# Kernel tuning notes

Hardware: AMD Instinct MI355X
Metric: run time of the kernel (lower is better)

## Reference

```python
import jax, jax.numpy as jnp
import numpy as np
import math

B, N, C, H = 4, 8192, 256, 8
D = C // H
EPS = 1e-6

def _ln(x, g, b):
    m = jnp.mean(x, -1, keepdims=True)
    v = jnp.mean((x - m) ** 2, -1, keepdims=True)
    return (x - m) * jax.lax.rsqrt(v + EPS) * g + b

def _pe(n, c):
    # sinusoidal PE, sin at even dims, cos at odd dims
    pos = jnp.arange(n, dtype=jnp.float32)[:, None]
    div = jnp.exp(jnp.arange(0, c, 2, dtype=jnp.float32) * (-math.log(10000.0) / c))
    ang = pos * div  # [n, c//2]
    return jnp.stack([jnp.sin(ang), jnp.cos(ang)], axis=-1).reshape(n, c)

def _heads(t):
    b, n, _ = t.shape
    return t.reshape(b, n, H, D).transpose(0, 2, 1, 3)  # [B,H,N,D]

def _forward(input, fx, Input_f, ln1_g, ln1_b, ln2_g, ln2_b, ln3_g, ln3_b,
             Wq, bq, Wk0, bk0, Wv0, bv0, Wk1, bk1, Wv1, bv1, Wo, bo,
             Wm1, bm1, Wm2, bm2, mu):
    pe = _pe(N, C)
    x = input + pe
    f = Input_f + pe
    x = _ln(x, ln1_g, ln1_b)
    f = _ln(f, ln2_g, ln2_b)
    # LinearCrossAttention: query from f; (key,value) streams = [f, x]
    q = jax.nn.softmax(_heads(f @ Wq + bq), axis=-1)  # [B,H,N,D]
    out = q
    for src, Wk, bk, Wv, bv in ((f, Wk0, bk0, Wv0, bv0), (x, Wk1, bk1, Wv1, bv1)):
        k = jax.nn.softmax(_heads(src @ Wk + bk), axis=-1)
        v = _heads(src @ Wv + bv)
        kv = jnp.einsum('bhnd,bhne->bhde', k, v)   # [B,H,D,D] small
        ksum = jnp.sum(k, axis=2)                  # [B,H,D]
        d_inv = 1.0 / jnp.einsum('bhnd,bhd->bhn', q, ksum)[..., None]
        out = out + jnp.einsum('bhnd,bhde->bhne', q, kv) * d_inv
    out = out.transpose(0, 2, 1, 3).reshape(out.shape[0], N, C)
    x = out @ Wo + bo + input          # residual
    y = _ln(x, ln3_g, ln3_b)
    y = jax.nn.gelu(y @ Wm1 + bm1, approximate=False) @ Wm2 + bm2
    x = x + y
    # bilinear low-rank fx update without n x n matrix
    xtfx = jnp.einsum('bnc,bnf->bcf', x, fx)
    fx_new = jnp.einsum('bnc,bcf->bnf', x * jax.nn.softplus(mu), xtfx)
    fx_new = jnp.where(fx_new >= 0, fx_new, 0.01 * fx_new)  # LeakyReLU(0.01)
    return x, fx_new

def setup_inputs() -> dict:
    key = jax.random.key(0)
    ks = jax.random.split(key, 16)
    w = lambda i: jax.random.normal(ks[i], (C, C), jnp.float32) * 0.02
    z = jnp.zeros((C,), jnp.float32)
    o = jnp.ones((C,), jnp.float32)
    return {
        'input': jax.random.normal(ks[0], (B, N, C), jnp.float32),
        'fx': jax.random.normal(ks[1], (B, N, C), jnp.float32),
        'Input_f': jax.random.normal(ks[2], (B, N, C), jnp.float32),
        'ln1_g': o, 'ln1_b': z, 'ln2_g': o, 'ln2_b': z, 'ln3_g': o, 'ln3_b': z,
        'Wq': w(3), 'bq': z,
        'Wk0': w(4), 'bk0': z, 'Wv0': w(5), 'bv0': z,
        'Wk1': w(6), 'bk1': z, 'Wv1': w(7), 'bv1': z,
        'Wo': w(8), 'bo': z,
        'Wm1': w(9), 'bm1': z, 'Wm2': w(10), 'bm2': z,
        'mu': z,
    }

def reference(input, fx, Input_f, ln1_g, ln1_b, ln2_g, ln2_b, ln3_g, ln3_b,
              Wq, bq, Wk0, bk0, Wv0, bv0, Wk1, bk1, Wv1, bv1, Wo, bo,
              Wm1, bm1, Wm2, bm2, mu):
    return _forward(input, fx, Input_f, ln1_g, ln1_b, ln2_g, ln2_b, ln3_g, ln3_b,
                    Wq, bq, Wk0, bk0, Wv0, bv0, Wk1, bk1, Wv1, bv1, Wo, bo,
                    Wm1, bm1, Wm2, bm2, mu)
```

## Files before the change

kernel.cpp:

```cpp
#include <hip/hip_runtime.h>


typedef __attribute__((ext_vector_type(8))) short    bf16x8;
typedef __attribute__((ext_vector_type(4))) float    f32x4;
typedef __attribute__((ext_vector_type(8))) unsigned short ushortx8;
typedef __attribute__((ext_vector_type(4))) unsigned short ushortx4;

static constexpr int Bn = 4, Nn = 8192, Cn = 256, Hn = 8, Dn = 32;
static constexpr int BN = Bn * Nn;
static constexpr long long S = (long long)BN * Cn;

#define DEVI __device__ __forceinline__

#define GLOAD_LDS16(gsrc, ldst)                                                  \
    __builtin_amdgcn_global_load_lds(                                            \
        (const __attribute__((address_space(1))) unsigned int*)(gsrc),           \
        (__attribute__((address_space(3))) unsigned int*)(ldst), 16, 0, 0)

DEVI unsigned short f2bf(float f) {
    unsigned int u = __builtin_bit_cast(unsigned int, f);
    u += 0x7fffu + ((u >> 16) & 1u);
    return (unsigned short)(u >> 16);
}
DEVI float bf2f(unsigned short h) {
    unsigned int u = ((unsigned int)h) << 16;
    return __builtin_bit_cast(float, u);
}

__global__ __launch_bounds__(256) void wtrans_all_kernel(
    const float* __restrict__ W0, const float* __restrict__ W1,
    const float* __restrict__ W2, const float* __restrict__ W3,
    const float* __restrict__ W4, const float* __restrict__ W5,
    const float* __restrict__ W6, const float* __restrict__ W7,
    unsigned short* __restrict__ WtAll) {
    __shared__ float tile[256][33];
    const float* W;
    switch (blockIdx.y) {
        case 0: W = W0; break; case 1: W = W1; break;
        case 2: W = W2; break; case 3: W = W3; break;
        case 4: W = W4; break; case 5: W = W5; break;
        case 6: W = W6; break; default: W = W7; break;
    }
    unsigned short* Wt = WtAll + (size_t)blockIdx.y * 65536;
    int t = threadIdx.x;
    int j0 = blockIdx.x * 32;
#pragma unroll
    for (int p = 0; p < 32; ++p) {
        int k = p * 8 + (t >> 5);
        tile[k][t & 31] = W[k * Cn + j0 + (t & 31)];
    }
    __syncthreads();
#pragma unroll
    for (int p = 0; p < 8; ++p) {
        int j = p * 4 + (t >> 6);
        int k0 = (t & 63) * 4;
        ushortx4 o;
        o.x = f2bf(tile[k0 + 0][j]);
        o.y = f2bf(tile[k0 + 1][j]);
        o.z = f2bf(tile[k0 + 2][j]);
        o.w = f2bf(tile[k0 + 3][j]);
        *(ushortx4*)(Wt + (long long)(j0 + j) * Cn + k0) = o;
    }
}

__global__ __launch_bounds__(256) void peln2_kernel(
    const float* __restrict__ in0, const float* __restrict__ g0, const float* __restrict__ b0,
    unsigned short* __restrict__ o0,
    const float* __restrict__ in1, const float* __restrict__ g1, const float* __restrict__ b1,
    unsigned short* __restrict__ o1) {
    const float* in  = blockIdx.y ? in1 : in0;
    const float* gam = blockIdx.y ? g1 : g0;
    const float* bet = blockIdx.y ? b1 : b0;
    unsigned short* outb = blockIdx.y ? o1 : o0;
    int r = blockIdx.x * 4 + (threadIdx.x >> 6);
    int lane = threadIdx.x & 63;
    int n = r & (Nn - 1);
    int c0 = lane * 4;
    const float* rowp = in + (long long)r * Cn + c0;
    float v0 = rowp[0], v1 = rowp[1], v2 = rowp[2], v3 = rowp[3];
    const float Kf = 0.07195578415606394f;
    float fn = (float)n;
    float ang0 = fn * expf(-Kf * (float)(2 * lane));
    float ang1 = fn * expf(-Kf * (float)(2 * lane + 1));
    v0 += sinf(ang0); v1 += cosf(ang0);
    v2 += sinf(ang1); v3 += cosf(ang1);
    float s = v0 + v1 + v2 + v3;
#pragma unroll
    for (int m = 1; m < 64; m <<= 1) s += __shfl_xor(s, m, 64);
    float mean = s * (1.0f / 256.0f);
    float d0 = v0 - mean, d1 = v1 - mean, d2 = v2 - mean, d3 = v3 - mean;
    float q = d0 * d0 + d1 * d1 + d2 * d2 + d3 * d3;
#pragma unroll
    for (int m = 1; m < 64; m <<= 1) q += __shfl_xor(q, m, 64);
    float rstd = rsqrtf(q * (1.0f / 256.0f) + 1e-6f);
    float4 g4 = *(const float4*)(gam + c0);
    float4 b4 = *(const float4*)(bet + c0);
    ushortx4 o;
    o.x = f2bf(d0 * rstd * g4.x + b4.x);
    o.y = f2bf(d1 * rstd * g4.y + b4.y);
    o.z = f2bf(d2 * rstd * g4.z + b4.z);
    o.w = f2bf(d3 * rstd * g4.w + b4.w);
    *(ushortx4*)(outb + (long long)r * Cn + c0) = o;
}

__global__ __launch_bounds__(256) void ln_kernel(const float* __restrict__ in,
                                                 const float* __restrict__ gam,
                                                 const float* __restrict__ bet,
                                                 unsigned short* __restrict__ outb) {
    int r = blockIdx.x * 4 + (threadIdx.x >> 6);
    int lane = threadIdx.x & 63;
    int c0 = lane * 4;
    const float* rowp = in + (long long)r * Cn + c0;
    float v0 = rowp[0], v1 = rowp[1], v2 = rowp[2], v3 = rowp[3];
    float s = v0 + v1 + v2 + v3;
#pragma unroll
    for (int m = 1; m < 64; m <<= 1) s += __shfl_xor(s, m, 64);
    float mean = s * (1.0f / 256.0f);
    float d0 = v0 - mean, d1 = v1 - mean, d2 = v2 - mean, d3 = v3 - mean;
    float q = d0 * d0 + d1 * d1 + d2 * d2 + d3 * d3;
#pragma unroll
    for (int m = 1; m < 64; m <<= 1) q += __shfl_xor(q, m, 64);
    float rstd = rsqrtf(q * (1.0f / 256.0f) + 1e-6f);
    float4 g4 = *(const float4*)(gam + c0);
    float4 b4 = *(const float4*)(bet + c0);
    ushortx4 o;
    o.x = f2bf(d0 * rstd * g4.x + b4.x);
    o.y = f2bf(d1 * rstd * g4.y + b4.y);
    o.z = f2bf(d2 * rstd * g4.z + b4.z);
    o.w = f2bf(d3 * rstd * g4.w + b4.w);
    *(ushortx4*)(outb + (long long)r * Cn + c0) = o;
}

__global__ __launch_bounds__(256, 4) void qkv_gemm_kernel(
    const unsigned short* __restrict__ A0, const unsigned short* __restrict__ A1,
    const unsigned short* __restrict__ WtAll,
    const float* __restrict__ bq, const float* __restrict__ bk0,
    const float* __restrict__ bv0, const float* __restrict__ bk1,
    const float* __restrict__ bv1,
    unsigned short* __restrict__ qb, unsigned short* __restrict__ kb0,
    unsigned short* __restrict__ vb0, unsigned short* __restrict__ kb1,
    unsigned short* __restrict__ vb1,
    float* __restrict__ ks0, float* __restrict__ ks1) {
    __shared__ unsigned short As[2][128][64];
    int t = threadIdx.x;
    int row0 = blockIdx.x * 128;
    int y = blockIdx.y;

    const unsigned short* A;
    const unsigned short* Btw;
    const float* bsel; unsigned short* osel; bool sm; float* ksp;
    int colIn;
    if (y < 12) {
        A = A0; int wid = y >> 2; colIn = (y & 3) * 64;
        Btw = WtAll + (size_t)wid * 65536;
        if (wid == 0)      { bsel = bq;  osel = qb;  sm = true;  ksp = nullptr; }
        else if (wid == 1) { bsel = bk0; osel = kb0; sm = true;  ksp = ks0; }
        else               { bsel = bv0; osel = vb0; sm = false; ksp = nullptr; }
    } else {
        int y2 = y - 12;
        A = A1; int wid = y2 >> 2; colIn = (y2 & 3) * 64;
        Btw = WtAll + (size_t)(3 + wid) * 65536;
        if (wid == 0)      { bsel = bk1; osel = kb1; sm = true;  ksp = ks1; }
        else               { bsel = bv1; osel = vb1; sm = false; ksp = nullptr; }
    }

    int lane = t & 63, w = t >> 6;
    int wr = w >> 1, wc = w & 1;
    int frow = lane & 15, fk = (lane >> 4) * 8;

    bf16x8 bfr[4][2][2];
#pragma unroll
    for (int kt = 0; kt < 4; ++kt)
#pragma unroll
        for (int ks = 0; ks < 2; ++ks)
#pragma unroll
            for (int n = 0; n < 2; ++n)
                bfr[kt][ks][n] = *(const bf16x8*)(
                    Btw + (long long)(colIn + wc * 32 + n * 16 + frow) * Cn
                        + kt * 64 + ks * 32 + fk);

    int srow_in_g = lane >> 3;
    int schunk = lane & 7;
    auto stageA = [&](int kt, int bf) {
#pragma unroll
        for (int i = 0; i < 4; ++i) {
            int g = w * 4 + i;
            int r = g * 8 + srow_in_g;
            int c = schunk ^ (r & 7);
            const unsigned short* src = A + (long long)(row0 + r) * Cn + kt * 64 + c * 8;
            GLOAD_LDS16(src, &As[bf][g * 8][0]);
        }
    };

    f32x4 acc[4][2];
#pragma unroll
    for (int m = 0; m < 4; ++m)
#pragma unroll
        for (int n = 0; n < 2; ++n) {
            acc[m][n][0] = 0.f; acc[m][n][1] = 0.f;
            acc[m][n][2] = 0.f; acc[m][n][3] = 0.f;
        }

    stageA(0, 0);
    int bf = 0;
#pragma unroll
    for (int kt = 0; kt < 4; ++kt) {
        if (kt < 3) {
            stageA(kt + 1, bf ^ 1);
            asm volatile("s_waitcnt vmcnt(4)" ::: "memory");
        } else {
            asm volatile("s_waitcnt vmcnt(0)" ::: "memory");
        }
        __builtin_amdgcn_s_barrier();
#pragma unroll
        for (int ks = 0; ks < 2; ++ks) {
#pragma unroll
            for (int m = 0; m < 4; ++m) {
                int arow = wr * 64 + m * 16 + frow;
                bf16x8 afr = *(const bf16x8*)&As[bf][arow][(ks * 32 + fk) ^ ((arow & 7) << 3)];
#pragma unroll
                for (int n = 0; n < 2; ++n)
                    acc[m][n] = __builtin_amdgcn_mfma_f32_16x16x32_bf16(afr, bfr[kt][ks][n],
                                                                        acc[m][n], 0, 0, 0);
            }
        }
        __builtin_amdgcn_s_barrier();
        bf ^= 1;
    }

    if (sm) {
        int colA = colIn + wc * 32 + frow;
        float b0 = bsel[colA], b1 = bsel[colA + 16];
        float ps0 = 0.f, ps1 = 0.f;
#pragma unroll
        for (int m = 0; m < 4; ++m) {
            int rbase = row0 + wr * 64 + m * 16 + (lane >> 4) * 4;
#pragma unroll
            for (int r = 0; r < 4; ++r) {
                float e0 = __expf(acc[m][0][r] + b0);
                float e1 = __expf(acc[m][1][r] + b1);
                float ssum = e0 + e1;
#pragma unroll
                for (int msk = 1; msk < 16; msk <<= 1) ssum += __shfl_xor(ssum, msk);
                float inv = 1.0f / ssum;
                e0 *= inv; e1 *= inv;
                long long idx = (long long)(rbase + r) * Cn + colA;
                osel[idx] = f2bf(e0);
                osel[idx + 16] = f2bf(e1);
                ps0 += e0; ps1 += e1;
            }
        }
        if (ksp) {
            ps0 += __shfl_xor(ps0, 16); ps0 += __shfl_xor(ps0, 32);
            ps1 += __shfl_xor(ps1, 16); ps1 += __shfl_xor(ps1, 32);
            if (lane < 16) {
                int b = row0 >> 13;
                atomicAdd(ksp + (b * 8 + (colA >> 5)) * 32 + (colA & 31), ps0);
                int c2 = colA + 16;
                atomicAdd(ksp + (b * 8 + (c2 >> 5)) * 32 + (c2 & 31), ps1);
            }
        }
    } else {
#pragma unroll
        for (int m = 0; m < 4; ++m) {
            int rbase = row0 + wr * 64 + m * 16 + (lane >> 4) * 4;
#pragma unroll
            for (int n = 0; n < 2; ++n) {
                int col = colIn + wc * 32 + n * 16 + frow;
                float bv = bsel[col];
#pragma unroll
                for (int r = 0; r < 4; ++r) {
                    long long idx = (long long)(rbase + r) * Cn + col;
                    osel[idx] = f2bf(acc[m][n][r] + bv);
                }
            }
        }
    }
}

template <int EPI>
__global__ __launch_bounds__(256, 4) void gemm_kernel(
    const unsigned short* __restrict__ A, const unsigned short* __restrict__ Bt,
    const float* __restrict__ bias, float* __restrict__ outF,
    const float* __restrict__ resid, unsigned short* __restrict__ outB,
    unsigned short* __restrict__ outB2, const float* __restrict__ mu) {
    __shared__ unsigned short As[2][128][64];
    int t = threadIdx.x;
    int row0 = blockIdx.x * 128;
    int col0 = blockIdx.y * 64;
    if (EPI == 4) Bt += (size_t)(row0 >> 13) * Cn * Cn;
    int lane = t & 63, w = t >> 6;
    int wr = w >> 1, wc = w & 1;
    int frow = lane & 15, fk = (lane >> 4) * 8;

    bf16x8 bfr[4][2][2];
#pragma unroll
    for (int kt = 0; kt < 4; ++kt)
#pragma unroll
        for (int ks = 0; ks < 2; ++ks)
#pragma unroll
            for (int n = 0; n < 2; ++n)
                bfr[kt][ks][n] = *(const bf16x8*)(
                    Bt + (long long)(col0 + wc * 32 + n * 16 + frow) * Cn
                       + kt * 64 + ks * 32 + fk);

    int srow_in_g = lane >> 3;
    int schunk = lane & 7;
    auto stageA = [&](int kt, int bf) {
#pragma unroll
        for (int i = 0; i < 4; ++i) {
            int g = w * 4 + i;
            int r = g * 8 + srow_in_g;
            int c = schunk ^ (r & 7);
            const unsigned short* src = A + (long long)(row0 + r) * Cn + kt * 64 + c * 8;
            GLOAD_LDS16(src, &As[bf][g * 8][0]);
        }
    };

    f32x4 acc[4][2];
#pragma unroll
    for (int m = 0; m < 4; ++m)
#pragma unroll
        for (int n = 0; n < 2; ++n) {
            acc[m][n][0] = 0.f; acc[m][n][1] = 0.f;
            acc[m][n][2] = 0.f; acc[m][n][3] = 0.f;
        }

    stageA(0, 0);
    int bf = 0;
#pragma unroll
    for (int kt = 0; kt < 4; ++kt) {
        if (kt < 3) {
            stageA(kt + 1, bf ^ 1);
            asm volatile("s_waitcnt vmcnt(4)" ::: "memory");
        } else {
            asm volatile("s_waitcnt vmcnt(0)" ::: "memory");
        }
        __builtin_amdgcn_s_barrier();
#pragma unroll
        for (int ks = 0; ks < 2; ++ks) {
#pragma unroll
            for (int m = 0; m < 4; ++m) {
                int arow = wr * 64 + m * 16 + frow;
                bf16x8 afr = *(const bf16x8*)&As[bf][arow][(ks * 32 + fk) ^ ((arow & 7) << 3)];
#pragma unroll
                for (int n = 0; n < 2; ++n)
                    acc[m][n] = __builtin_amdgcn_mfma_f32_16x16x32_bf16(afr, bfr[kt][ks][n],
                                                                        acc[m][n], 0, 0, 0);
            }
        }
        __builtin_amdgcn_s_barrier();
        bf ^= 1;
    }

    float spv[2];
    if (EPI == 3) {
#pragma unroll
        for (int n = 0; n < 2; ++n) {
            float m_ = mu[col0 + wc * 32 + n * 16 + frow];
            spv[n] = (m_ > 20.f) ? m_ : log1pf(expf(m_));
        }
    }
#pragma unroll
    for (int m = 0; m < 4; ++m) {
        int rbase = row0 + wr * 64 + m * 16 + (lane >> 4) * 4;
#pragma unroll
        for (int n = 0; n < 2; ++n) {
            int col = col0 + wc * 32 + n * 16 + frow;
            float bv = (EPI == 4) ? 0.0f : bias[col];
#pragma unroll
            for (int r = 0; r < 4; ++r) {
                long long idx = (long long)(rbase + r) * Cn + col;
                float v = acc[m][n][r] + bv;
                if (EPI == 0) {
                    outB[idx] = f2bf(v);
                } else if (EPI == 1) {
                    float sg = 1.0f / (1.0f + __expf(-1.702f * v));
                    outB[idx] = f2bf(v * sg);
                } else if (EPI == 2) {
                    outF[idx] = v + resid[idx];
                } else if (EPI == 3) {
                    float xv = v + resid[idx];
                    outF[idx] = xv;
                    outB2[idx] = f2bf(xv * spv[n]);
                } else {
                    outF[idx] = (v >= 0.0f) ? v : 0.01f * v;
                }
            }
        }
    }
}

__global__ __launch_bounds__(256) void kv_gemm_kernel(
    const unsigned short* __restrict__ kbs0, const unsigned short* __restrict__ vbs0,
    float* __restrict__ kv0p,
    const unsigned short* __restrict__ kbs1, const unsigned short* __restrict__ vbs1,
    float* __restrict__ kv1p) {
    const unsigned short* kb = blockIdx.z ? kbs1 : kbs0;
    const unsigned short* vb = blockIdx.z ? vbs1 : vbs0;
    float* kv = blockIdx.z ? kv1p : kv0p;
    __shared__ unsigned short kl[256][36];
    __shared__ unsigned short vl[256][36];
    __shared__ float red[4][1024];
    int bh = blockIdx.x, b = bh >> 3, h = bh & 7;
    int n0 = blockIdx.y * 256;
    int t = threadIdx.x, lane = t & 63, w = t >> 6;
    {
        int r0 = t >> 2, ch = (t & 3) * 8;
        long long gbase = ((long long)(b * Nn + n0)) * Cn + h * Dn + ch;
#pragma unroll
        for (int i = 0; i < 4; ++i) {
            int r = r0 + i * 64;
            ushortx8 dk = *(const ushortx8*)(kb + gbase + (long long)r * Cn);
            ushortx8 dv = *(const ushortx8*)(vb + gbase + (long long)r * Cn);
            ushortx4 k0 = {dk[0], dk[1], dk[2], dk[3]};
            ushortx4 k1 = {dk[4], dk[5], dk[6], dk[7]};
            ushortx4 v0 = {dv[0], dv[1], dv[2], dv[3]};
            ushortx4 v1 = {dv[4], dv[5], dv[6], dv[7]};
            *(ushortx4*)&kl[r][ch]     = k0;
            *(ushortx4*)&kl[r][ch + 4] = k1;
            *(ushortx4*)&vl[r][ch]     = v0;
            *(ushortx4*)&vl[r][ch + 4] = v1;
        }
    }
    __syncthreads();
    int frow = lane & 15, fk = (lane >> 4) * 8;
    f32x4 acc[2][2];
#pragma unroll
    for (int m = 0; m < 2; ++m)
#pragma unroll
        for (int n = 0; n < 2; ++n) {
            acc[m][n][0] = 0.f; acc[m][n][1] = 0.f;
            acc[m][n][2] = 0.f; acc[m][n][3] = 0.f;
        }
    int nb = w * 64;
#pragma unroll
    for (int s = 0; s < 2; ++s) {
        int kk = nb + s * 32 + fk;
        bf16x8 a0, a1, b0, b1;
#pragma unroll
        for (int j = 0; j < 8; ++j) {
            a0[j] = (short)kl[kk + j][frow];
            a1[j] = (short)kl[kk + j][16 + frow];
            b0[j] = (short)vl[kk + j][frow];
            b1[j] = (short)vl[kk + j][16 + frow];
        }
        acc[0][0] = __builtin_amdgcn_mfma_f32_16x16x32_bf16(a0, b0, acc[0][0], 0, 0, 0);
        acc[0][1] = __builtin_amdgcn_mfma_f32_16x16x32_bf16(a0, b1, acc[0][1], 0, 0, 0);
        acc[1][0] = __builtin_amdgcn_mfma_f32_16x16x32_bf16(a1, b0, acc[1][0], 0, 0, 0);
        acc[1][1] = __builtin_amdgcn_mfma_f32_16x16x32_bf16(a1, b1, acc[1][1], 0, 0, 0);
    }
#pragma unroll
    for (int m = 0; m < 2; ++m)
#pragma unroll
        for (int n = 0; n < 2; ++n)
#pragma unroll
            for (int r = 0; r < 4; ++r)
                red[w][(m * 16 + (lane >> 4) * 4 + r) * 32 + n * 16 + frow] = acc[m][n][r];
    __syncthreads();
    float* out = kv + (long long)bh * 1024;
#pragma unroll
    for (int i = 0; i < 4; ++i) {
        int idx = t + i * 256;
        atomicAdd(out + idx, red[0][idx] + red[1][idx] + red[2][idx] + red[3][idx]);
    }
}

__global__ __launch_bounds__(256) void attn_out_kernel(
    const unsigned short* __restrict__ qb, const float* __restrict__ kv0,
    const float* __restrict__ ks0, const float* __restrict__ kv1,
    const float* __restrict__ ks1, unsigned short* __restrict__ outb) {
    __shared__ unsigned short BT[80][40];
    int bh = blockIdx.y;
    int b = bh >> 3, h = bh & 7;
    int n0 = blockIdx.x * 128;
    int t = threadIdx.x;
    {
        int e = t & 31, d0 = t >> 5;
        const float* KV0 = kv0 + (long long)bh * 1024;
        const float* KV1 = kv1 + (long long)bh * 1024;
#pragma unroll
        for (int i = 0; i < 4; ++i) {
            int d = d0 + 8 * i;
            BT[e][d]      = f2bf(KV0[d * 32 + e]);
            BT[32 + e][d] = f2bf(KV1[d * 32 + e]);
        }
        if (t < 32)            BT[64][t]      = f2bf(ks0[bh * 32 + t]);
        else if (t < 64)       BT[65][t - 32] = f2bf(ks1[bh * 32 + (t - 32)]);
        if (t < 224) {
            int c = 66 + (t >> 4), k2 = (t & 15) * 2;
            BT[c][k2] = 0; BT[c][k2 + 1] = 0;
        }
    }
    __syncthreads();

    int lane = t & 63, w = t >> 6;
    int frow = lane & 15, fk = (lane >> 4) * 8;
    bf16x8 bfr[5];
#pragma unroll
    for (int n = 0; n < 5; ++n)
        bfr[n] = *(const bf16x8*)&BT[n * 16 + frow][fk];

    f32x4 acc[2][5];
#pragma unroll
    for (int m = 0; m < 2; ++m)
#pragma unroll
        for (int n = 0; n < 5; ++n) {
            acc[m][n][0] = 0.f; acc[m][n][1] = 0.f;
            acc[m][n][2] = 0.f; acc[m][n][3] = 0.f;
        }
    long long grow0 = (long long)b * Nn + n0 + w * 32;
#pragma unroll
    for (int m = 0; m < 2; ++m) {
        bf16x8 afr = *(const bf16x8*)(qb + (grow0 + m * 16 + frow) * Cn + h * Dn + fk);
#pragma unroll
        for (int n = 0; n < 5; ++n)
            acc[m][n] = __builtin_amdgcn_mfma_f32_16x16x32_bf16(afr, bfr[n],
                                                                acc[m][n], 0, 0, 0);
    }
#pragma unroll
    for (int m = 0; m < 2; ++m) {
#pragma unroll
        for (int r = 0; r < 4; ++r) {
            float s0 = __shfl(acc[m][4][r], lane & 48, 64);
            float s1 = __shfl(acc[m][4][r], (lane & 48) + 1, 64);
            float inv0 = 1.0f / s0, inv1 = 1.0f / s1;
            long long row = grow0 + m * 16 + (lane >> 4) * 4 + r;
            long long base = row * Cn + h * Dn + (lane & 15);
            float q0 = bf2f(qb[base]), q1 = bf2f(qb[base + 16]);
            outb[base]      = f2bf(q0 + acc[m][0][r] * inv0 + acc[m][2][r] * inv1);
            outb[base + 16] = f2bf(q1 + acc[m][1][r] * inv0 + acc[m][3][r] * inv1);
        }
    }
}

__global__ __launch_bounds__(256) void transpose_cast_kernel(
    const float* __restrict__ in, unsigned short* __restrict__ out) {
    __shared__ float tile[64][33];
    int b = blockIdx.z;
    int n0 = blockIdx.x * 64;
    int c0 = blockIdx.y * 32;
    int t = threadIdx.x;
    int r = t >> 2;
    int cc = (t & 3) * 8;
    const float* src = in + ((long long)b * Nn + n0 + r) * Cn + c0 + cc;
    float4 a0 = *(const float4*)src;
    float4 a1 = *(const float4*)(src + 4);
    tile[r][cc + 0] = a0.x; tile[r][cc + 1] = a0.y;
    tile[r][cc + 2] = a0.z; tile[r][cc + 3] = a0.w;
    tile[r][cc + 4] = a1.x; tile[r][cc + 5] = a1.y;
    tile[r][cc + 6] = a1.z; tile[r][cc + 7] = a1.w;
    __syncthreads();
    int c = t >> 3;
    int nn = (t & 7) * 8;
    ushortx8 o;
#pragma unroll
    for (int j = 0; j < 8; ++j) o[j] = f2bf(tile[nn + j][c]);
    *(ushortx8*)(out + ((long long)b * Cn + c0 + c) * Nn + n0 + nn) = o;
}

__global__ __launch_bounds__(256, 2) void bilin_gemm_kernel(
    const unsigned short* __restrict__ A, const unsigned short* __restrict__ Bm,
    float* __restrict__ Cacc) {
    __shared__ unsigned short As[128][72];
    __shared__ unsigned short Bs[64][72];
    int t = threadIdx.x;
    int b = blockIdx.z >> 4;
    int split = blockIdx.z & 15;
    int row0 = blockIdx.x * 128;
    int col0 = blockIdx.y * 64;
    const unsigned short* Ab = A + (long long)b * Cn * Nn;
    const unsigned short* Bb = Bm + (long long)b * Cn * Nn;
    int lane = t & 63, w = t >> 6;
    int wr = w >> 1, wc = w & 1;
    int frow = lane & 15, fk = (lane >> 4) * 8;
    f32x4 acc[4][2];
#pragma unroll
    for (int m = 0; m < 4; ++m)
#pragma unroll
        for (int n = 0; n < 2; ++n) {
            acc[m][n][0] = 0.f; acc[m][n][1] = 0.f;
            acc[m][n][2] = 0.f; acc[m][n][3] = 0.f;
        }
    int sr = t >> 3, sc = (t & 7) * 8;
    for (int kt = 0; kt < 8; ++kt) {
        int k0 = split * 512 + kt * 64;
#pragma unroll
        for (int p = 0; p < 4; ++p) {
            int rr = sr + p * 32;
            ushortx8 d = *(const ushortx8*)(Ab + (long long)(row0 + rr) * Nn + k0 + sc);
            *(ushortx8*)&As[rr][sc] = d;
        }
#pragma unroll
        for (int p = 0; p < 2; ++p) {
            int br = sr + p * 32;
            ushortx8 d = *(const ushortx8*)(Bb + (long long)(col0 + br) * Nn + k0 + sc);
            *(ushortx8*)&Bs[br][sc] = d;
        }
        __syncthreads();
#pragma unroll
        for (int ks = 0; ks < 2; ++ks) {
            bf16x8 bfr[2];
#pragma unroll
            for (int n = 0; n < 2; ++n)
                bfr[n] = *(const bf16x8*)&Bs[wc * 32 + n * 16 + frow][ks * 32 + fk];
#pragma unroll
            for (int m = 0; m < 4; ++m) {
                bf16x8 afr = *(const bf16x8*)&As[wr * 64 + m * 16 + frow][ks * 32 + fk];
#pragma unroll
                for (int n = 0; n < 2; ++n)
                    acc[m][n] = __builtin_amdgcn_mfma_f32_16x16x32_bf16(afr, bfr[n],
                                                                        acc[m][n], 0, 0, 0);
            }
        }
        __syncthreads();
    }
    float* base = Cacc + (long long)b * Cn * Cn;
#pragma unroll
    for (int m = 0; m < 4; ++m) {
        int rbase = row0 + wr * 64 + m * 16 + (lane >> 4) * 4;
#pragma unroll
        for (int n = 0; n < 2; ++n) {
            int col = col0 + wc * 32 + n * 16 + frow;
#pragma unroll
            for (int r = 0; r < 4; ++r)
                atomicAdd(base + (long long)(rbase + r) * Cn + col, acc[m][n][r]);
        }
    }
}

__global__ __launch_bounds__(256) void castf2b_kernel(const float* __restrict__ in,
                                                      unsigned short* __restrict__ out) {
    int i = (blockIdx.x * 256 + threadIdx.x) * 4;
    float4 v = *(const float4*)(in + i);
    ushortx4 o;
    o.x = f2bf(v.x); o.y = f2bf(v.y); o.z = f2bf(v.z); o.w = f2bf(v.w);
    *(ushortx4*)(out + i) = o;
}

extern "C" void kernel_launch(void* const* d_in, const int* in_sizes, int n_in,
                              void* d_out, int out_size, void* d_ws, size_t ws_size,
                              hipStream_t stream) {
    const float* input  = (const float*)d_in[0];
    const float* fx     = (const float*)d_in[1];
    const float* inputf = (const float*)d_in[2];
    const float* ln1g = (const float*)d_in[3],  *ln1b = (const float*)d_in[4];
    const float* ln2g = (const float*)d_in[5],  *ln2b = (const float*)d_in[6];
    const float* ln3g = (const float*)d_in[7],  *ln3b = (const float*)d_in[8];
    const float* Wq  = (const float*)d_in[9],   *bq  = (const float*)d_in[10];
    const float* Wk0 = (const float*)d_in[11],  *bk0 = (const float*)d_in[12];
    const float* Wv0 = (const float*)d_in[13],  *bv0 = (const float*)d_in[14];
    const float* Wk1 = (const float*)d_in[15],  *bk1 = (const float*)d_in[16];
    const float* Wv1 = (const float*)d_in[17],  *bv1 = (const float*)d_in[18];
    const float* Wo  = (const float*)d_in[19],  *bo  = (const float*)d_in[20];
    const float* Wm1 = (const float*)d_in[21],  *bm1 = (const float*)d_in[22];
    const float* Wm2 = (const float*)d_in[23],  *bm2 = (const float*)d_in[24];
    const float* mu  = (const float*)d_in[25];

    float* xOut  = (float*)d_out;
    float* fxOut = xOut + S;

    char* ws = (char*)d_ws;
    const size_t SB = (size_t)S * 2;
    unsigned short* x1b  = (unsigned short*)(ws + 0 * SB);
    unsigned short* f1b  = (unsigned short*)(ws + 1 * SB);
    unsigned short* qb   = (unsigned short*)(ws + 2 * SB);
    unsigned short* kb   = (unsigned short*)(ws + 3 * SB);
    unsigned short* vb   = (unsigned short*)(ws + 4 * SB);
    unsigned short* outb = (unsigned short*)(ws + 5 * SB);
    unsigned short* kb2  = (unsigned short*)(ws + 6 * SB);
    unsigned short* vb2  = (unsigned short*)(ws + 7 * SB);
    unsigned short* Wt   = (unsigned short*)(ws + 8 * SB);
    unsigned short* xtT  = (unsigned short*)(ws + 8 * SB + (size_t)8 * 65536 * 2);
    float* zbase = (float*)(ws + 8 * SB + (size_t)8 * 65536 * 2 + (size_t)Bn * 65536 * 2);
    float* kv0   = zbase;
    float* kv1   = zbase + 32768;
    float* ks0   = zbase + 65536;
    float* ks1   = zbase + 66560;
    float* xtfxT = zbase + 67584;
    const size_t ZFLOATS = 67584 + 262144;

    hipMemsetAsync(zbase, 0, ZFLOATS * sizeof(float), stream);

    wtrans_all_kernel<<<dim3(8, 8), 256, 0, stream>>>(Wq, Wk0, Wv0, Wk1, Wv1, Wo, Wm1, Wm2, Wt);

    peln2_kernel<<<dim3(BN / 4, 2), 256, 0, stream>>>(input, ln1g, ln1b, x1b,
                                                      inputf, ln2g, ln2b, f1b);

    qkv_gemm_kernel<<<dim3(BN / 128, 20), 256, 0, stream>>>(
        f1b, x1b, Wt, bq, bk0, bv0, bk1, bv1,
        qb, kb, vb, kb2, vb2, ks0, ks1);
    kv_gemm_kernel<<<dim3(32, 32, 2), 256, 0, stream>>>(kb, vb, kv0, kb2, vb2, kv1);

    attn_out_kernel<<<dim3(Nn / 128, Bn * Hn), 256, 0, stream>>>(qb, kv0, ks0, kv1, ks1, outb);

    dim3 ggrid(BN / 128, 4);
    gemm_kernel<2><<<ggrid, 256, 0, stream>>>(outb, Wt + (size_t)5 * 65536, bo,
                                              xOut, input, nullptr, nullptr, nullptr);
    ln_kernel<<<BN / 4, 256, 0, stream>>>(xOut, ln3g, ln3b, f1b);
    gemm_kernel<1><<<ggrid, 256, 0, stream>>>(f1b, Wt + (size_t)6 * 65536, bm1,
                                              nullptr, nullptr, x1b, nullptr, nullptr);
    gemm_kernel<3><<<ggrid, 256, 0, stream>>>(x1b, Wt + (size_t)7 * 65536, bm2,
                                              xOut, xOut, nullptr, qb, mu);

    transpose_cast_kernel<<<dim3(Nn / 64, Cn / 32, Bn), 256, 0, stream>>>(xOut, kb);
    transpose_cast_kernel<<<dim3(Nn / 64, Cn / 32, Bn), 256, 0, stream>>>(fx,   vb);
    bilin_gemm_kernel<<<dim3(2, 4, 64), 256, 0, stream>>>(vb, kb, xtfxT);
    castf2b_kernel<<<(int)(Bn * 65536 / 1024), 256, 0, stream>>>(xtfxT, xtT);
    gemm_kernel<4><<<ggrid, 256, 0, stream>>>(qb, xtT, nullptr,
                                              fxOut, nullptr, nullptr, nullptr, nullptr);
}
```

Before: 278.1 us.

## Widen QKV GEMM output tile to 128 columns to halve activation reloads

Each QKV GEMM block now computes 128 output columns instead of 64, so each warp holds a 4x4 accumulator grid and the grid's y dimension shrinks from 20 to 10. The point is to cut how often each A row-tile is re-streamed from memory, roughly halving activation read traffic. Weight fragments are no longer preloaded into registers for all k-steps; they are now loaded from global memory inside the k-loop, which can expose load latency. The softmax epilogue is extended to cover two heads per warp. Launch bounds drop to 3 waves to make room for the larger accumulator.

```diff
diff --git a/kernel.cpp b/kernel.cpp
--- a/kernel.cpp
+++ b/kernel.cpp
@@ -131,7 +131,7 @@
     *(ushortx4*)(outb + (long long)r * Cn + c0) = o;
 }
 
-__global__ __launch_bounds__(256, 4) void qkv_gemm_kernel(
+__global__ __launch_bounds__(256, 3) void qkv_gemm_kernel(
     const unsigned short* __restrict__ A0, const unsigned short* __restrict__ A1,
     const unsigned short* __restrict__ WtAll,
     const float* __restrict__ bq, const float* __restrict__ bk0,
@@ -150,15 +150,15 @@
     const unsigned short* Btw;
     const float* bsel; unsigned short* osel; bool sm; float* ksp;
     int colIn;
-    if (y < 12) {
-        A = A0; int wid = y >> 2; colIn = (y & 3) * 64;
+    if (y < 6) {
+        A = A0; int wid = y >> 1; colIn = (y & 1) * 128;
         Btw = WtAll + (size_t)wid * 65536;
         if (wid == 0)      { bsel = bq;  osel = qb;  sm = true;  ksp = nullptr; }
         else if (wid == 1) { bsel = bk0; osel = kb0; sm = true;  ksp = ks0; }
         else               { bsel = bv0; osel = vb0; sm = false; ksp = nullptr; }
     } else {
-        int y2 = y - 12;
-        A = A1; int wid = y2 >> 2; colIn = (y2 & 3) * 64;
+        int y2 = y - 6;
+        A = A1; int wid = y2 >> 1; colIn = (y2 & 1) * 128;
         Btw = WtAll + (size_t)(3 + wid) * 65536;
         if (wid == 0)      { bsel = bk1; osel = kb1; sm = true;  ksp = ks1; }
         else               { bsel = bv1; osel = vb1; sm = false; ksp = nullptr; }
@@ -167,17 +167,6 @@
     int lane = t & 63, w = t >> 6;
     int wr = w >> 1, wc = w & 1;
     int frow = lane & 15, fk = (lane >> 4) * 8;
-
-    bf16x8 bfr[4][2][2];
-#pragma unroll
-    for (int kt = 0; kt < 4; ++kt)
-#pragma unroll
-        for (int ks = 0; ks < 2; ++ks)
-#pragma unroll
-            for (int n = 0; n < 2; ++n)
-                bfr[kt][ks][n] = *(const bf16x8*)(
-                    Btw + (long long)(colIn + wc * 32 + n * 16 + frow) * Cn
-                        + kt * 64 + ks * 32 + fk);
 
     int srow_in_g = lane >> 3;
     int schunk = lane & 7;
@@ -192,11 +181,11 @@
         }
     };
 
-    f32x4 acc[4][2];
+    f32x4 acc[4][4];
 #pragma unroll
     for (int m = 0; m < 4; ++m)
 #pragma unroll
-        for (int n = 0; n < 2; ++n) {
+        for (int n = 0; n < 4; ++n) {
             acc[m][n][0] = 0.f; acc[m][n][1] = 0.f;
             acc[m][n][2] = 0.f; acc[m][n][3] = 0.f;
         }
@@ -205,6 +194,14 @@
     int bf = 0;
 #pragma unroll
     for (int kt = 0; kt < 4; ++kt) {
+        bf16x8 bfr[2][4];
+#pragma unroll
+        for (int ks = 0; ks < 2; ++ks)
+#pragma unroll
+            for (int n = 0; n < 4; ++n)
+                bfr[ks][n] = *(const bf16x8*)(
+                    Btw + (long long)(colIn + wc * 64 + n * 16 + frow) * Cn
+                        + kt * 64 + ks * 32 + fk);
         if (kt < 3) {
             stageA(kt + 1, bf ^ 1);
             asm volatile("s_waitcnt vmcnt(4)" ::: "memory");
@@ -219,8 +216,8 @@
                 int arow = wr * 64 + m * 16 + frow;
                 bf16x8 afr = *(const bf16x8*)&As[bf][arow][(ks * 32 + fk) ^ ((arow & 7) << 3)];
 #pragma unroll
-                for (int n = 0; n < 2; ++n)
-                    acc[m][n] = __builtin_amdgcn_mfma_f32_16x16x32_bf16(afr, bfr[kt][ks][n],
+                for (int n = 0; n < 4; ++n)
+                    acc[m][n] = __builtin_amdgcn_mfma_f32_16x16x32_bf16(afr, bfr[ks][n],
                                                                         acc[m][n], 0, 0, 0);
             }
         }
@@ -229,9 +226,10 @@
     }
 
     if (sm) {
-        int colA = colIn + wc * 32 + frow;
+        int colA = colIn + wc * 64 + frow;
         float b0 = bsel[colA], b1 = bsel[colA + 16];
-        float ps0 = 0.f, ps1 = 0.f;
+        float b2 = bsel[colA + 32], b3 = bsel[colA + 48];
+        float ps0 = 0.f, ps1 = 0.f, ps2 = 0.f, ps3 = 0.f;
 #pragma unroll
         for (int m = 0; m < 4; ++m) {
             int rbase = row0 + wr * 64 + m * 16 + (lane >> 4) * 4;
@@ -239,25 +237,36 @@
             for (int r = 0; r < 4; ++r) {
                 float e0 = __expf(acc[m][0][r] + b0);
                 float e1 = __expf(acc[m][1][r] + b1);
-                float ssum = e0 + e1;
-#pragma unroll
-                for (int msk = 1; msk < 16; msk <<= 1) ssum += __shfl_xor(ssum, msk);
-                float inv = 1.0f / ssum;
-                e0 *= inv; e1 *= inv;
+                float e2 = __expf(acc[m][2][r] + b2);
+                float e3 = __expf(acc[m][3][r] + b3);
+                float s01 = e0 + e1, s23 = e2 + e3;
+#pragma unroll
+                for (int msk = 1; msk < 16; msk <<= 1) {
+                    s01 += __shfl_xor(s01, msk);
+                    s23 += __shfl_xor(s23, msk);
+                }
+                float i01 = 1.0f / s01, i23 = 1.0f / s23;
+                e0 *= i01; e1 *= i01; e2 *= i23; e3 *= i23;
                 long long idx = (long long)(rbase + r) * Cn + colA;
-                osel[idx] = f2bf(e0);
+                osel[idx]      = f2bf(e0);
                 osel[idx + 16] = f2bf(e1);
-                ps0 += e0; ps1 += e1;
+                osel[idx + 32] = f2bf(e2);
+                osel[idx + 48] = f2bf(e3);
+                ps0 += e0; ps1 += e1; ps2 += e2; ps3 += e3;
             }
         }
         if (ksp) {
             ps0 += __shfl_xor(ps0, 16); ps0 += __shfl_xor(ps0, 32);
             ps1 += __shfl_xor(ps1, 16); ps1 += __shfl_xor(ps1, 32);
+            ps2 += __shfl_xor(ps2, 16); ps2 += __shfl_xor(ps2, 32);
+            ps3 += __shfl_xor(ps3, 16); ps3 += __shfl_xor(ps3, 32);
             if (lane < 16) {
                 int b = row0 >> 13;
-                atomicAdd(ksp + (b * 8 + (colA >> 5)) * 32 + (colA & 31), ps0);
-                int c2 = colA + 16;
-                atomicAdd(ksp + (b * 8 + (c2 >> 5)) * 32 + (c2 & 31), ps1);
+                int c0a = colA, c1a = colA + 16, c2a = colA + 32, c3a = colA + 48;
+                atomicAdd(ksp + (b * 8 + (c0a >> 5)) * 32 + (c0a & 31), ps0);
+                atomicAdd(ksp + (b * 8 + (c1a >> 5)) * 32 + (c1a & 31), ps1);
+                atomicAdd(ksp + (b * 8 + (c2a >> 5)) * 32 + (c2a & 31), ps2);
+                atomicAdd(ksp + (b * 8 + (c3a >> 5)) * 32 + (c3a & 31), ps3);
             }
         }
     } else {
@@ -265,8 +274,8 @@
         for (int m = 0; m < 4; ++m) {
             int rbase = row0 + wr * 64 + m * 16 + (lane >> 4) * 4;
 #pragma unroll
-            for (int n = 0; n < 2; ++n) {
-                int col = colIn + wc * 32 + n * 16 + frow;
+            for (int n = 0; n < 4; ++n) {
+                int col = colIn + wc * 64 + n * 16 + frow;
                 float bv = bsel[col];
 #pragma unroll
                 for (int r = 0; r < 4; ++r) {
@@ -687,7 +696,7 @@
     peln2_kernel<<<dim3(BN / 4, 2), 256, 0, stream>>>(input, ln1g, ln1b, x1b,
                                                       inputf, ln2g, ln2b, f1b);
 
-    qkv_gemm_kernel<<<dim3(BN / 128, 20), 256, 0, stream>>>(
+    qkv_gemm_kernel<<<dim3(BN / 128, 10), 256, 0, stream>>>(
         f1b, x1b, Wt, bq, bk0, bv0, bk1, bv1,
         qb, kb, vb, kb2, vb2, ks0, ks1);
     kv_gemm_kernel<<<dim3(32, 32, 2), 256, 0, stream>>>(kb, vb, kv0, kb2, vb2, kv1);
```

New measurement: 270.9 us. 1.03x faster.
